# Optimization experiments

Measured on AMD Instinct MI355X. Metric: run time of the kernel, lower is better.

The kernel has to match this reference:

```python
import jax, jax.numpy as jnp
import numpy as np

EPS = 1e-6  # clamp for arccos domain (matches typical GeodesicLoss eps)


def _random_rotations(key, n):
    # Orthonormalize random matrices into proper rotations (stand-in for
    # the gemmi symmetry operators of 'P 61 2 2', S=12 ops).
    A = jax.random.normal(key, (n, 3, 3), dtype=jnp.float32)
    Q, R = jnp.linalg.qr(A)
    # fix signs so det = +1
    d = jnp.sign(jnp.diagonal(R, axis1=-2, axis2=-1))
    Q = Q * d[:, None, :]
    det = jnp.linalg.det(Q)
    Q = Q.at[:, :, 0].multiply(det[:, None])
    return Q


def setup_inputs() -> dict:
    key = jax.random.key(0)
    k1, k2, k3 = jax.random.split(key, 3)
    B, C, S = 32768, 64, 12
    R_pred = _random_rotations(k1, B * C).reshape(B, C, 3, 3)
    R_gt = _random_rotations(k2, B)
    rot_mats = _random_rotations(k3, S)
    return {"R_pred": R_pred, "R_gt": R_gt, "rot_mats": rot_mats}


def reference(R_pred, R_gt, rot_mats):
    # R_gt_sym[b,s] = rot_mats[s] @ R_gt[b]  -> (B, S, 3, 3)
    R_gt_sym = jnp.einsum('sij,bjk->bsik', rot_mats, R_gt)
    # geodesic loss: arccos((trace(R_pred @ R_gt_sym^T) - 1) / 2)
    # trace(A @ B^T) = sum_ij A_ij * B_ij  -> avoids materializing (B,C,S,3,3)
    tr = jnp.einsum('bcij,bsij->bcs', R_pred, R_gt_sym)
    cos = jnp.clip((tr - 1.0) * 0.5, -1.0 + EPS, 1.0 - EPS)
    all_losses = jnp.arccos(cos)            # (B, C, S)
    min_loss_sym = jnp.min(all_losses, axis=2)   # min over symmetry ops
    best_candidate = jnp.min(min_loss_sym, axis=1)  # min over candidates
    return best_candidate.mean()
```

## Files before the change

kernel.cpp:

```cpp
#include <hip/hip_runtime.h>
#include <math.h>

#define EPS_CLIP 1e-6f
#define WPB 4
#define NWAVES 4

struct F3 { float x, y, z; };

template <int SS>
__global__ __launch_bounds__(256) void sym_loss_kernel(
    const float* __restrict__ R_pred,
    const float* __restrict__ R_gt,
    const float* __restrict__ rot,
    float* __restrict__ partial,
    int S_rt)
{
    const int S    = SS ? SS : S_rt;
    const int tid  = threadIdx.x;
    const int lane = tid & 63;
    const int wid  = tid >> 6;
    const int gw   = __builtin_amdgcn_readfirstlane(blockIdx.x * NWAVES + wid);
    const int b0   = gw * WPB;

    const F3* base = reinterpret_cast<const F3*>(R_pred) + ((size_t)b0 * 64 + lane) * 3;

    F3 A[3][3];
    #pragma unroll
    for (int r = 0; r < 3; ++r) A[0][r] = base[r];
    #pragma unroll
    for (int r = 0; r < 3; ++r) A[1][r] = base[192 + r];

    float mk[WPB];
    #pragma unroll
    for (int k = 0; k < WPB; ++k) {
        if (k + 2 < WPB) {
            #pragma unroll
            for (int r = 0; r < 3; ++r)
                A[(k + 2) % 3][r] = base[(size_t)(k + 2) * 192 + r];
        }
        const int slot = k % 3;
        const int b = b0 + k;

        const float* G = R_gt + (size_t)b * 9;
        float g[9];
        #pragma unroll
        for (int e = 0; e < 9; ++e) g[e] = G[e];

        const float p[9] = { A[slot][0].x, A[slot][0].y, A[slot][0].z,
                             A[slot][1].x, A[slot][1].y, A[slot][1].z,
                             A[slot][2].x, A[slot][2].y, A[slot][2].z };

        float q[9];
        #pragma unroll
        for (int i = 0; i < 3; ++i)
            #pragma unroll
            for (int j = 0; j < 3; ++j)
                q[i * 3 + j] = fmaf(p[i * 3 + 0], g[j * 3 + 0],
                               fmaf(p[i * 3 + 1], g[j * 3 + 1],
                                    p[i * 3 + 2] * g[j * 3 + 2]));

        float m = -1e30f;
        if (SS) {
            #pragma unroll
            for (int s = 0; s < SS; ++s) {
                const float* Rs = rot + s * 9;
                float tr = 0.f;
                #pragma unroll
                for (int e = 0; e < 9; ++e) tr = fmaf(q[e], Rs[e], tr);
                m = fmaxf(m, tr);
            }
        } else {
            for (int s = 0; s < S; ++s) {
                const float* Rs = rot + s * 9;
                float tr = 0.f;
                #pragma unroll
                for (int e = 0; e < 9; ++e) tr = fmaf(q[e], Rs[e], tr);
                m = fmaxf(m, tr);
            }
        }

        #pragma unroll
        for (int off = 32; off; off >>= 1) m = fmaxf(m, __shfl_xor(m, off));
        mk[k] = m;
    }

    float mv = mk[0];
    #pragma unroll
    for (int k = 1; k < WPB; ++k) mv = (lane == k) ? mk[k] : mv;
    float cosv = (mv - 1.0f) * 0.5f;
    cosv = fminf(fmaxf(cosv, -1.0f + EPS_CLIP), 1.0f - EPS_CLIP);
    float a = (lane < WPB) ? acosf(cosv) : 0.0f;
    a += __shfl_xor(a, 1);
    a += __shfl_xor(a, 2);

    __shared__ float sLoss[NWAVES];
    if (lane == 0) sLoss[wid] = a;
    __syncthreads();
    if (tid == 0) {
        float sum = 0.f;
        #pragma unroll
        for (int i = 0; i < NWAVES; ++i) sum += sLoss[i];
        partial[blockIdx.x] = sum;
    }
}

__global__ __launch_bounds__(1024) void reduce_kernel(
    const float* __restrict__ partial, int n, float* __restrict__ out, float invB)
{
    float sum = 0.f;
    for (int i = threadIdx.x; i < n; i += 1024) sum += partial[i];
    #pragma unroll
    for (int off = 32; off; off >>= 1) sum += __shfl_xor(sum, off);
    __shared__ float ws[16];
    const int w = threadIdx.x >> 6;
    if ((threadIdx.x & 63) == 0) ws[w] = sum;
    __syncthreads();
    if (threadIdx.x == 0) {
        float t = 0.f;
        #pragma unroll
        for (int i = 0; i < 16; ++i) t += ws[i];
        out[0] = t * invB;
    }
}

extern "C" void kernel_launch(void* const* d_in, const int* in_sizes, int n_in,
                              void* d_out, int out_size, void* d_ws, size_t ws_size,
                              hipStream_t stream) {
    const float* R_pred = (const float*)d_in[0];
    const float* R_gt   = (const float*)d_in[1];
    const float* rot    = (const float*)d_in[2];
    float* out = (float*)d_out;

    const int B = in_sizes[1] / 9;
    const int S = in_sizes[2] / 9;
    const int nBlocks = B / (WPB * NWAVES);

    float* partial = (float*)d_ws;

    if (S == 12)
        sym_loss_kernel<12><<<nBlocks, 256, 0, stream>>>(R_pred, R_gt, rot, partial, S);
    else
        sym_loss_kernel<0><<<nBlocks, 256, 0, stream>>>(R_pred, R_gt, rot, partial, S);

    reduce_kernel<<<1, 1024, 0, stream>>>(partial, nBlocks, out, 1.0f / (float)B);
}
```

Measured before the change: 21.53 us.

## Stage R_pred through LDS with coalesced float4 loads and packed FMA traces

Each wave now loads a candidate batch of R_pred with fully coalesced float4 loads, writes it to shared memory, and reads back each lane's 9 elements. This replaces strided 12-byte per-lane loads and prefetches the next batch into registers. The 12 symmetry traces now use packed 2-wide FMAs to cut VALU instruction count. The cost is extra LDS traffic, likely bank conflicts on the stride-9 reads, and no barrier between the LDS write and read.

```diff
diff --git a/kernel.cpp b/kernel.cpp
--- a/kernel.cpp
+++ b/kernel.cpp
@@ -5,7 +5,15 @@
 #define WPB 4
 #define NWAVES 4
 
-struct F3 { float x, y, z; };
+typedef float v2f __attribute__((ext_vector_type(2)));
+
+#if __has_builtin(__builtin_elementwise_fma)
+#define PK_FMA(a, b, c) __builtin_elementwise_fma((a), (b), (c))
+#else
+static __device__ __forceinline__ v2f PK_FMA(v2f a, v2f b, v2f c) {
+    v2f r; r.x = fmaf(a.x, b.x, c.x); r.y = fmaf(a.y, b.y, c.y); return r;
+}
+#endif
 
 template <int SS>
 __global__ __launch_bounds__(256) void sym_loss_kernel(
@@ -22,33 +30,38 @@
     const int gw   = __builtin_amdgcn_readfirstlane(blockIdx.x * NWAVES + wid);
     const int b0   = gw * WPB;
 
-    const F3* base = reinterpret_cast<const F3*>(R_pred) + ((size_t)b0 * 64 + lane) * 3;
+    __shared__ float tile[NWAVES][576];
+    float* __restrict__ T = tile[wid];
 
-    F3 A[3][3];
-    #pragma unroll
-    for (int r = 0; r < 3; ++r) A[0][r] = base[r];
-    #pragma unroll
-    for (int r = 0; r < 3; ++r) A[1][r] = base[192 + r];
+    const float* wsrc = R_pred + (size_t)b0 * 576;
+
+    float4 ra = *reinterpret_cast<const float4*>(wsrc + 4 * lane);
+    float4 rb = *reinterpret_cast<const float4*>(wsrc + 256 + 4 * lane);
+    float  rc = wsrc[512 + lane];
 
     float mk[WPB];
     #pragma unroll
     for (int k = 0; k < WPB; ++k) {
-        if (k + 2 < WPB) {
-            #pragma unroll
-            for (int r = 0; r < 3; ++r)
-                A[(k + 2) % 3][r] = base[(size_t)(k + 2) * 192 + r];
+        *reinterpret_cast<float4*>(T + 4 * lane)       = ra;
+        *reinterpret_cast<float4*>(T + 256 + 4 * lane) = rb;
+        T[512 + lane] = rc;
+
+        if (k + 1 < WPB) {
+            const float* nsrc = wsrc + (size_t)(k + 1) * 576;
+            ra = *reinterpret_cast<const float4*>(nsrc + 4 * lane);
+            rb = *reinterpret_cast<const float4*>(nsrc + 256 + 4 * lane);
+            rc = nsrc[512 + lane];
         }
-        const int slot = k % 3;
+
+        float p[9];
+        #pragma unroll
+        for (int e = 0; e < 9; ++e) p[e] = T[9 * lane + e];
+
         const int b = b0 + k;
-
         const float* G = R_gt + (size_t)b * 9;
         float g[9];
         #pragma unroll
         for (int e = 0; e < 9; ++e) g[e] = G[e];
-
-        const float p[9] = { A[slot][0].x, A[slot][0].y, A[slot][0].z,
-                             A[slot][1].x, A[slot][1].y, A[slot][1].z,
-                             A[slot][2].x, A[slot][2].y, A[slot][2].z };
 
         float q[9];
         #pragma unroll
@@ -59,14 +72,22 @@
                                fmaf(p[i * 3 + 1], g[j * 3 + 1],
                                     p[i * 3 + 2] * g[j * 3 + 2]));
 
+        const v2f q01 = {q[0], q[1]}, q23 = {q[2], q[3]},
+                  q45 = {q[4], q[5]}, q67 = {q[6], q[7]};
+        const float q8 = q[8];
+
         float m = -1e30f;
         if (SS) {
             #pragma unroll
             for (int s = 0; s < SS; ++s) {
                 const float* Rs = rot + s * 9;
-                float tr = 0.f;
-                #pragma unroll
-                for (int e = 0; e < 9; ++e) tr = fmaf(q[e], Rs[e], tr);
+                const v2f r01 = {Rs[0], Rs[1]}, r23 = {Rs[2], Rs[3]},
+                          r45 = {Rs[4], Rs[5]}, r67 = {Rs[6], Rs[7]};
+                v2f acc = q01 * r01;
+                acc = PK_FMA(q23, r23, acc);
+                acc = PK_FMA(q45, r45, acc);
+                acc = PK_FMA(q67, r67, acc);
+                const float tr = fmaf(q8, Rs[8], acc.x + acc.y);
                 m = fmaxf(m, tr);
             }
         } else {
```

After: 25.01 us. 1.16x slower.
